# Kernel optimization log

Measured on AMD Instinct MI355X. Metric: run time of the kernel, lower is better.

## Reference

```python
import jax, jax.numpy as jnp
import numpy as np

N_NODES = 100000
N_EDGES = 1600000
D_IN = 128
D_OUT = 64


def setup_inputs() -> dict:
    key = jax.random.key(0)
    k1, k2, k3, k4, k5 = jax.random.split(key, 5)
    return {
        "input_feature": jax.random.normal(k1, (N_NODES, D_IN), dtype=jnp.float32),
        "weight": jax.random.normal(k2, (D_IN, D_OUT), dtype=jnp.float32) * (1.0 / np.sqrt(D_IN)),
        "bias": jnp.zeros((D_OUT,), dtype=jnp.float32),
        "adj_row": jax.random.randint(k3, (N_EDGES,), 0, N_NODES, dtype=jnp.int32),
        "adj_col": jax.random.randint(k4, (N_EDGES,), 0, N_NODES, dtype=jnp.int32),
        "adj_val": jax.random.uniform(k5, (N_EDGES,), dtype=jnp.float32),
    }


def reference(input_feature, weight, bias, adj_row, adj_col, adj_val):
    # support = X @ W  -> [N, D_OUT]
    support = input_feature @ weight
    # sparse adjacency matmul: out[i] = sum_e adj_val[e] * support[adj_col[e]] for adj_row[e] == i
    gathered = adj_val[:, None] * support[adj_col]  # [E, D_OUT]
    out = jax.ops.segment_sum(gathered, adj_row, num_segments=N_NODES)
    return out + bias
```

## Files before the change

### kernel.cpp

```cpp
#include <hip/hip_runtime.h>

constexpr int N_NODES = 100000;
constexpr int N_EDGES = 1600000;
constexpr int D_IN  = 128;
constexpr int D_OUT = 64;

constexpr int GEMM_BLOCKS = (N_NODES + 63) / 64;
constexpr int CHUNK = 4096;
constexpr int PBLK  = (N_EDGES + CHUNK - 1) / CHUNK;
constexpr int RPB   = 128;
constexpr int NBUCK = (N_NODES + RPB - 1) / RPB;
constexpr int NBPAD = 784;
constexpr int CAP_FINE = 2432;
constexpr int ESPAN = 128;
constexpr int NSPAN = N_EDGES / ESPAN;
constexpr int WT_STRIDE = 136;

typedef unsigned long long ull;
typedef unsigned short u16;
typedef unsigned int u32;
typedef __attribute__((ext_vector_type(8))) short short8;
typedef __attribute__((ext_vector_type(4))) float floatx4;

__device__ __forceinline__ u16 f32_to_bf16_rtn(float f) {
    u32 u = __float_as_uint(f);
    u32 r = u + 0x7FFFu + ((u >> 16) & 1u);
    return (u16)(r >> 16);
}

__global__ __launch_bounds__(256) void prep_kernel(const float* __restrict__ X,
                                                   const float* __restrict__ W,
                                                   u16* __restrict__ S,
                                                   const int* __restrict__ adj_row,
                                                   u32* __restrict__ H) {
    __shared__ u16 smem[64 * WT_STRIDE];

    if (blockIdx.x >= GEMM_BLOCKS) {
        u32* cnt = (u32*)smem;
        const int b = blockIdx.x - GEMM_BLOCKS;
        const int t = threadIdx.x;
        for (int i = t; i < NBUCK; i += 256) cnt[i] = 0;
        __syncthreads();
        const int base = b * CHUNK;
        #pragma unroll
        for (int j = 0; j < CHUNK / 256; ++j) {
            int e = base + t + j * 256;
            if (e < N_EDGES) atomicAdd(&cnt[(u32)adj_row[e] >> 7], 1u);
        }
        __syncthreads();
        for (int i = t; i < NBUCK; i += 256) H[b * NBUCK + i] = cnt[i];
        return;
    }

    u16* Wt = smem;
    for (int i = threadIdx.x; i < D_IN * D_OUT; i += 256) {
        int k = i >> 6, n = i & 63;
        Wt[n * WT_STRIDE + k] = f32_to_bf16_rtn(W[i]);
    }
    __syncthreads();

    const int lane = threadIdx.x & 63;
    const int wv   = threadIdx.x >> 6;
    const int m0   = blockIdx.x * 64 + wv * 16;
    const int mr   = lane & 15;
    const int q    = lane >> 4;
    int mrow = m0 + mr; if (mrow >= N_NODES) mrow = N_NODES - 1;
    const float* xb = X + mrow * D_IN + q * 8;

    floatx4 acc0 = 0, acc1 = 0, acc2 = 0, acc3 = 0;

    #pragma unroll
    for (int kt = 0; kt < 4; ++kt) {
        float4 xa = *(const float4*)(xb + kt * 32);
        float4 xc = *(const float4*)(xb + kt * 32 + 4);
        union { short8 v; u16 u[8]; } A;
        A.u[0] = f32_to_bf16_rtn(xa.x); A.u[1] = f32_to_bf16_rtn(xa.y);
        A.u[2] = f32_to_bf16_rtn(xa.z); A.u[3] = f32_to_bf16_rtn(xa.w);
        A.u[4] = f32_to_bf16_rtn(xc.x); A.u[5] = f32_to_bf16_rtn(xc.y);
        A.u[6] = f32_to_bf16_rtn(xc.z); A.u[7] = f32_to_bf16_rtn(xc.w);

        const u16* wrow = &Wt[mr * WT_STRIDE + kt * 32 + q * 8];
        short8 b0 = *(const short8*)(wrow + 0 * 16 * WT_STRIDE);
        short8 b1 = *(const short8*)(wrow + 1 * 16 * WT_STRIDE);
        short8 b2 = *(const short8*)(wrow + 2 * 16 * WT_STRIDE);
        short8 b3 = *(const short8*)(wrow + 3 * 16 * WT_STRIDE);
        acc0 = __builtin_amdgcn_mfma_f32_16x16x32_bf16(A.v, b0, acc0, 0, 0, 0);
        acc1 = __builtin_amdgcn_mfma_f32_16x16x32_bf16(A.v, b1, acc1, 0, 0, 0);
        acc2 = __builtin_amdgcn_mfma_f32_16x16x32_bf16(A.v, b2, acc2, 0, 0, 0);
        acc3 = __builtin_amdgcn_mfma_f32_16x16x32_bf16(A.v, b3, acc3, 0, 0, 0);
    }

    #pragma unroll
    for (int reg = 0; reg < 4; ++reg) {
        int rr = m0 + q * 4 + reg;
        if (rr < N_NODES) {
            u16* sp = &S[rr * D_OUT + mr];
            sp[0]  = f32_to_bf16_rtn(acc0[reg]);
            sp[16] = f32_to_bf16_rtn(acc1[reg]);
            sp[32] = f32_to_bf16_rtn(acc2[reg]);
            sp[48] = f32_to_bf16_rtn(acc3[reg]);
        }
    }
}

__global__ __launch_bounds__(512) void scan1_kernel(u32* __restrict__ H,
                                                    u32* __restrict__ total) {
    __shared__ u32 wsum[8];
    const int k = blockIdx.x;
    const int t = threadIdx.x, lane = t & 63, w = t >> 6;
    u32 v = (t < PBLK) ? H[t * NBUCK + k] : 0;
    u32 incl = v;
    #pragma unroll
    for (int off = 1; off < 64; off <<= 1) {
        u32 u = __shfl_up(incl, off);
        if (lane >= off) incl += u;
    }
    if (lane == 63) wsum[w] = incl;
    __syncthreads();
    u32 wb = 0;
    for (int i = 0; i < w; ++i) wb += wsum[i];
    if (t < PBLK) H[t * NBUCK + k] = wb + incl - v;
    if (t == 511) total[k] = wb + incl;
}

__global__ __launch_bounds__(1024) void scan2_kernel(const u32* __restrict__ total,
                                                     u32* __restrict__ bucketStart) {
    __shared__ u32 wsum[16];
    const int t = threadIdx.x, lane = t & 63, w = t >> 6;
    u32 v = (t < NBUCK) ? total[t] : 0;
    u32 incl = v;
    #pragma unroll
    for (int off = 1; off < 64; off <<= 1) {
        u32 u = __shfl_up(incl, off);
        if (lane >= off) incl += u;
    }
    if (lane == 63) wsum[w] = incl;
    __syncthreads();
    u32 wb = 0;
    for (int i = 0; i < w; ++i) wb += wsum[i];
    if (t < NBUCK) bucketStart[t] = wb + incl - v;
    if (t == NBUCK - 1) bucketStart[NBUCK] = wb + incl;
}

__global__ __launch_bounds__(1024) void coarse_kernel(const int* __restrict__ adj_row,
                                                      const int* __restrict__ adj_col,
                                                      const float* __restrict__ adj_val,
                                                      const u32* __restrict__ H,
                                                      const u32* __restrict__ total,
                                                      const u32* __restrict__ bucketStart,
                                                      ull* __restrict__ edges) {
    __shared__ ull srt[CHUNK];
    __shared__ u32 lofs[NBPAD];
    __shared__ u32 cur[NBPAD];
    __shared__ u32 bp[NBUCK];
    __shared__ u32 wsum[4];

    const int b = blockIdx.x, t = threadIdx.x;
    const int base = b * CHUNK;
    const int nrec = (base + CHUNK <= N_EDGES) ? CHUNK : (N_EDGES - base);
    const bool last = (b == PBLK - 1);

    for (int i = t; i < NBPAD; i += 1024) {
        u32 c = 0;
        if (i < NBUCK) {
            u32 h0 = H[b * NBUCK + i];
            u32 h1 = last ? total[i] : H[(b + 1) * NBUCK + i];
            c = h1 - h0;
            bp[i] = bucketStart[i] + h0;
        }
        cur[i] = c;
    }
    __syncthreads();

    {
        const int lane = t & 63, w = t >> 6;
        u32 c0 = 0, c1 = 0, c2 = 0, c3 = 0, s = 0;
        if (t < NBPAD / 4) {
            c0 = cur[4 * t + 0]; c1 = cur[4 * t + 1];
            c2 = cur[4 * t + 2]; c3 = cur[4 * t + 3];
            s = c0 + c1 + c2 + c3;
        }
        u32 incl = s;
        #pragma unroll
        for (int off = 1; off < 64; off <<= 1) {
            u32 u = __shfl_up(incl, off);
            if (lane >= off) incl += u;
        }
        if (lane == 63 && w < 4) wsum[w] = incl;
        __syncthreads();
        if (t < NBPAD / 4) {
            u32 wb = 0;
            for (int i = 0; i < w; ++i) wb += wsum[i];
            u32 excl = wb + incl - s;
            lofs[4 * t + 0] = excl;
            lofs[4 * t + 1] = excl + c0;
            lofs[4 * t + 2] = excl + c0 + c1;
            lofs[4 * t + 3] = excl + c0 + c1 + c2;
            cur[4 * t + 0] = lofs[4 * t + 0];
            cur[4 * t + 1] = lofs[4 * t + 1];
            cur[4 * t + 2] = lofs[4 * t + 2];
            cur[4 * t + 3] = lofs[4 * t + 3];
        }
    }
    __syncthreads();

    #pragma unroll
    for (int j = 0; j < CHUNK / 1024; ++j) {
        int e = base + t + j * 1024;
        if (e < N_EDGES) {
            u32 row = (u32)adj_row[e];
            u32 p = atomicAdd(&cur[row >> 7], 1u);
            ull rec = ((ull)f32_to_bf16_rtn(adj_val[e]) << 48)
                    | ((ull)row << 17) | (u32)adj_col[e];
            srt[p] = rec;
        }
    }
    __syncthreads();

    for (int p = t; p < nrec; p += 1024) {
        ull rec = srt[p];
        u32 row = (u32)(rec >> 17) & 0x1FFFFu;
        u32 k = row >> 7;
        edges[bp[k] + (p - lofs[k])] = rec;
    }
}

__global__ __launch_bounds__(512) void fine_kernel(const u32* __restrict__ bucketStart,
                                                   ull* __restrict__ edges,
                                                   const float* __restrict__ bias,
                                                   float* __restrict__ out) {
    __shared__ ull srt[CAP_FINE];
    __shared__ u32 h[RPB], lofs[RPB], cur[RPB];

    const int k = blockIdx.x, t = threadIdx.x;
    const int gbeg = (int)bucketStart[k], gend = (int)bucketStart[k + 1];
    const int len = gend - gbeg;

    if (t < RPB) h[t] = 0;
    __syncthreads();

    ull r[5];
    int cnt = 0;
    for (int i = t; i < len && cnt < 5; i += 512) {
        r[cnt] = edges[gbeg + i];
        atomicAdd(&h[(u32)(r[cnt] >> 17) & 127u], 1u);
        ++cnt;
    }
    __syncthreads();

    if (t < 64) {
        u32 v0 = h[t], v1 = h[t + 64];
        u32 i0 = v0;
        #pragma unroll
        for (int off = 1; off < 64; off <<= 1) {
            u32 u = __shfl_up(i0, off);
            if (t >= off) i0 += u;
        }
        u32 t0 = __shfl(i0, 63);
        u32 i1 = v1;
        #pragma unroll
        for (int off = 1; off < 64; off <<= 1) {
            u32 u = __shfl_up(i1, off);
            if (t >= off) i1 += u;
        }
        i1 += t0;
        lofs[t] = i0 - v0;
        lofs[t + 64] = i1 - v1;
    }
    __syncthreads();

    if (t < RPB) cur[t] = lofs[t];
    __syncthreads();

    for (int c = 0; c < cnt; ++c) {
        u32 lrow = (u32)(r[c] >> 17) & 127u;
        u32 p = atomicAdd(&cur[lrow], 1u);
        if (p < CAP_FINE) srt[p] = r[c];
    }
    __syncthreads();

    const int lim = len < CAP_FINE ? len : CAP_FINE;
    for (int p = t; p < lim; p += 512) edges[gbeg + p] = srt[p];

    const float bv = bias[t & 63];
    const int rbase = k * RPB;
    for (int i = t; i < RPB * D_OUT; i += 512) {
        int row = rbase + (i >> 6);
        if (row < N_NODES) out[row * D_OUT + (i & 63)] = bv;
    }
}

__global__ __launch_bounds__(256) void gather_kernel(const ull* __restrict__ edges,
                                                     const u16* __restrict__ S,
                                                     const float* __restrict__ bias,
                                                     float* __restrict__ out) {
    const int lane = threadIdx.x & 63;
    const int wid  = __builtin_amdgcn_readfirstlane((blockIdx.x * 256 + threadIdx.x) >> 6);
    if (wid >= NSPAN) return;
    const float bv = bias[lane];

    int e = wid * ESPAN;
    const int eend = e + ESPAN;

    int currow;
    {
        ull m0 = edges[e];
        u32 lo = (u32)__builtin_amdgcn_readfirstlane((int)(u32)m0);
        u32 hi = (u32)__builtin_amdgcn_readfirstlane((int)(u32)(m0 >> 32));
        currow = (int)(((lo >> 17) | (hi << 15)) & 0x1FFFFu);
    }
    bool at_boundary = true;
    float acc = 0.f;

    while (e < eend) {
        ulonglong2 q0 = *(const ulonglong2*)(edges + e);
        ulonglong2 q1 = *(const ulonglong2*)(edges + e + 2);
        ulonglong2 q2 = *(const ulonglong2*)(edges + e + 4);
        ulonglong2 q3 = *(const ulonglong2*)(edges + e + 6);
        ull m[8] = { q0.x, q0.y, q1.x, q1.y, q2.x, q2.y, q3.x, q3.y };

        u32 lo[8], hi[8];
        #pragma unroll
        for (int j = 0; j < 8; ++j) {
            lo[j] = (u32)__builtin_amdgcn_readfirstlane((int)(u32)m[j]);
            hi[j] = (u32)__builtin_amdgcn_readfirstlane((int)(u32)(m[j] >> 32));
        }

        float sv[8];
        #pragma unroll
        for (int j = 0; j < 8; ++j) {
            u32 col = lo[j] & 0x1FFFFu;
            sv[j] = __uint_as_float((u32)S[col * D_OUT + lane] << 16);
        }

        #pragma unroll
        for (int j = 0; j < 8; ++j) {
            int r = (int)(((lo[j] >> 17) | (hi[j] << 15)) & 0x1FFFFu);
            if (r != currow) {
                if (at_boundary) atomicAdd(&out[currow * D_OUT + lane], acc);
                else             out[currow * D_OUT + lane] = acc + bv;
                currow = r; acc = 0.f; at_boundary = false;
            }
            float v = __uint_as_float(hi[j] & 0xFFFF0000u);
            acc += v * sv[j];
        }
        e += 8;
    }
    atomicAdd(&out[currow * D_OUT + lane], acc);
}

extern "C" void kernel_launch(void* const* d_in, const int* in_sizes, int n_in,
                              void* d_out, int out_size, void* d_ws, size_t ws_size,
                              hipStream_t stream) {
    const float* X    = (const float*)d_in[0];
    const float* W    = (const float*)d_in[1];
    const float* bias = (const float*)d_in[2];
    const int*   row  = (const int*)d_in[3];
    const int*   col  = (const int*)d_in[4];
    const float* val  = (const float*)d_in[5];
    float* out = (float*)d_out;

    char* ws = (char*)d_ws;
    u16*  S      = (u16*) (ws + 0);
    ull*  edges  = (ull*) (ws + 12800000);
    u32*  H      = (u32*) (ws + 25600000);
    u32*  total  = (u32*) (ws + 26823048);
    u32*  bstart = (u32*) (ws + 26826176);

    prep_kernel  <<<GEMM_BLOCKS + PBLK, 256, 0, stream>>>(X, W, S, row, H);
    scan1_kernel <<<NBUCK, 512, 0, stream>>>(H, total);
    scan2_kernel <<<1, 1024, 0, stream>>>(total, bstart);
    coarse_kernel<<<PBLK, 1024, 0, stream>>>(row, col, val, H, total, bstart, edges);
    fine_kernel  <<<NBUCK, 512, 0, stream>>>(bstart, edges, bias, out);
    gather_kernel<<<(NSPAN + 3) / 4, 256, 0, stream>>>(edges, S, bias, out);
}
```

Measured before the change: 188.5 us.

## Fuse fine sort and gather into per-bucket LDS accumulation kernel

Merges the fine-sort and gather kernels into one per-bucket kernel. After sorting a bucket's edges by row in shared memory, each wavefront accumulates whole rows straight from LDS and writes the output once with the bias added. This removes the write-back of sorted edges to global memory, the separate bias init of the output, the global atomics at span boundaries, and one kernel launch. In exchange there are fewer waves in flight per gather (8 waves per 128-row bucket), row lengths are uneven across waves, and edges past CAP_FINE are silently dropped.

```diff
diff --git a/kernel.cpp b/kernel.cpp
--- a/kernel.cpp
+++ b/kernel.cpp
@@ -12,8 +12,6 @@
 constexpr int NBUCK = (N_NODES + RPB - 1) / RPB;
 constexpr int NBPAD = 784;
 constexpr int CAP_FINE = 2432;
-constexpr int ESPAN = 128;
-constexpr int NSPAN = N_EDGES / ESPAN;
 constexpr int WT_STRIDE = 136;
 
 typedef unsigned long long ull;
@@ -225,14 +223,17 @@
     }
 }
 
-__global__ __launch_bounds__(512) void fine_kernel(const u32* __restrict__ bucketStart,
-                                                   ull* __restrict__ edges,
-                                                   const float* __restrict__ bias,
-                                                   float* __restrict__ out) {
+__global__ __launch_bounds__(512) void bucket_accum_kernel(const u32* __restrict__ bucketStart,
+                                                           const ull* __restrict__ edges,
+                                                           const u16* __restrict__ S,
+                                                           const float* __restrict__ bias,
+                                                           float* __restrict__ out) {
     __shared__ ull srt[CAP_FINE];
-    __shared__ u32 h[RPB], lofs[RPB], cur[RPB];
+    __shared__ u32 h[RPB], cur[RPB];
+    __shared__ u32 lofs[RPB + 1];
 
     const int k = blockIdx.x, t = threadIdx.x;
+    const int lane = t & 63, w = t >> 6;
     const int gbeg = (int)bucketStart[k], gend = (int)bucketStart[k + 1];
     const int len = gend - gbeg;
 
@@ -266,6 +267,7 @@
         i1 += t0;
         lofs[t] = i0 - v0;
         lofs[t + 64] = i1 - v1;
+        if (t == 0) lofs[RPB] = (u32)len;
     }
     __syncthreads();
 
@@ -279,74 +281,39 @@
     }
     __syncthreads();
 
-    const int lim = len < CAP_FINE ? len : CAP_FINE;
-    for (int p = t; p < lim; p += 512) edges[gbeg + p] = srt[p];
-
-    const float bv = bias[t & 63];
+    const float bv = bias[lane];
     const int rbase = k * RPB;
-    for (int i = t; i < RPB * D_OUT; i += 512) {
-        int row = rbase + (i >> 6);
-        if (row < N_NODES) out[row * D_OUT + (i & 63)] = bv;
-    }
-}
-
-__global__ __launch_bounds__(256) void gather_kernel(const ull* __restrict__ edges,
-                                                     const u16* __restrict__ S,
-                                                     const float* __restrict__ bias,
-                                                     float* __restrict__ out) {
-    const int lane = threadIdx.x & 63;
-    const int wid  = __builtin_amdgcn_readfirstlane((blockIdx.x * 256 + threadIdx.x) >> 6);
-    if (wid >= NSPAN) return;
-    const float bv = bias[lane];
-
-    int e = wid * ESPAN;
-    const int eend = e + ESPAN;
-
-    int currow;
-    {
-        ull m0 = edges[e];
-        u32 lo = (u32)__builtin_amdgcn_readfirstlane((int)(u32)m0);
-        u32 hi = (u32)__builtin_amdgcn_readfirstlane((int)(u32)(m0 >> 32));
-        currow = (int)(((lo >> 17) | (hi << 15)) & 0x1FFFFu);
-    }
-    bool at_boundary = true;
-    float acc = 0.f;
-
-    while (e < eend) {
-        ulonglong2 q0 = *(const ulonglong2*)(edges + e);
-        ulonglong2 q1 = *(const ulonglong2*)(edges + e + 2);
-        ulonglong2 q2 = *(const ulonglong2*)(edges + e + 4);
-        ulonglong2 q3 = *(const ulonglong2*)(edges + e + 6);
-        ull m[8] = { q0.x, q0.y, q1.x, q1.y, q2.x, q2.y, q3.x, q3.y };
-
-        u32 lo[8], hi[8];
-        #pragma unroll
-        for (int j = 0; j < 8; ++j) {
-            lo[j] = (u32)__builtin_amdgcn_readfirstlane((int)(u32)m[j]);
-            hi[j] = (u32)__builtin_amdgcn_readfirstlane((int)(u32)(m[j] >> 32));
-        }
-
-        float sv[8];
-        #pragma unroll
-        for (int j = 0; j < 8; ++j) {
-            u32 col = lo[j] & 0x1FFFFu;
-            sv[j] = __uint_as_float((u32)S[col * D_OUT + lane] << 16);
-        }
-
-        #pragma unroll
-        for (int j = 0; j < 8; ++j) {
-            int r = (int)(((lo[j] >> 17) | (hi[j] << 15)) & 0x1FFFFu);
-            if (r != currow) {
-                if (at_boundary) atomicAdd(&out[currow * D_OUT + lane], acc);
-                else             out[currow * D_OUT + lane] = acc + bv;
-                currow = r; acc = 0.f; at_boundary = false;
-            }
-            float v = __uint_as_float(hi[j] & 0xFFFF0000u);
-            acc += v * sv[j];
-        }
-        e += 8;
-    }
-    atomicAdd(&out[currow * D_OUT + lane], acc);
+    for (int rr = w; rr < RPB; rr += 8) {
+        const int row = rbase + rr;
+        if (row >= N_NODES) break;
+        int beg = (int)lofs[rr];
+        int end = (int)lofs[rr + 1];
+        if (end > CAP_FINE) end = CAP_FINE;
+        float acc = 0.f;
+        int e = beg;
+        for (; e + 4 <= end; e += 4) {
+            ull m0 = srt[e], m1 = srt[e + 1], m2 = srt[e + 2], m3 = srt[e + 3];
+            u32 c0 = (u32)m0 & 0x1FFFFu, c1 = (u32)m1 & 0x1FFFFu;
+            u32 c2 = (u32)m2 & 0x1FFFFu, c3 = (u32)m3 & 0x1FFFFu;
+            float s0 = __uint_as_float((u32)S[c0 * D_OUT + lane] << 16);
+            float s1 = __uint_as_float((u32)S[c1 * D_OUT + lane] << 16);
+            float s2 = __uint_as_float((u32)S[c2 * D_OUT + lane] << 16);
+            float s3 = __uint_as_float((u32)S[c3 * D_OUT + lane] << 16);
+            float v0 = __uint_as_float((u32)(m0 >> 32) & 0xFFFF0000u);
+            float v1 = __uint_as_float((u32)(m1 >> 32) & 0xFFFF0000u);
+            float v2 = __uint_as_float((u32)(m2 >> 32) & 0xFFFF0000u);
+            float v3 = __uint_as_float((u32)(m3 >> 32) & 0xFFFF0000u);
+            acc += v0 * s0; acc += v1 * s1; acc += v2 * s2; acc += v3 * s3;
+        }
+        for (; e < end; ++e) {
+            ull m0 = srt[e];
+            u32 c0 = (u32)m0 & 0x1FFFFu;
+            float s0 = __uint_as_float((u32)S[c0 * D_OUT + lane] << 16);
+            float v0 = __uint_as_float((u32)(m0 >> 32) & 0xFFFF0000u);
+            acc += v0 * s0;
+        }
+        out[row * D_OUT + lane] = acc + bv;
+    }
 }
 
 extern "C" void kernel_launch(void* const* d_in, const int* in_sizes, int n_in,
@@ -371,6 +338,5 @@
     scan1_kernel <<<NBUCK, 512, 0, stream>>>(H, total);
     scan2_kernel <<<1, 1024, 0, stream>>>(total, bstart);
     coarse_kernel<<<PBLK, 1024, 0, stream>>>(row, col, val, H, total, bstart, edges);
-    fine_kernel  <<<NBUCK, 512, 0, stream>>>(bstart, edges, bias, out);
-    gather_kernel<<<(NSPAN + 3) / 4, 256, 0, stream>>>(edges, S, bias, out);
-}
+    bucket_accum_kernel<<<NBUCK, 512, 0, stream>>>(bstart, edges, S, bias, out);
+}
```

Result: no change. 189.0 us (+0.3%).
